# Optimization experiments

Measured on AMD Instinct MI355X. Metric: run time of the kernel, lower is better.

The kernel has to match this reference:

```python
import jax, jax.numpy as jnp
import numpy as np

KL_W = 0.001
Q_W = 0.1

def setup_inputs() -> dict:
    key = jax.random.key(0)
    k1, k2, k3, k4 = jax.random.split(key, 4)
    B, N, M, L = 2, 4096, 4096, 512
    return {
        'pred': jax.random.normal(k1, (B, N, 3), dtype=jnp.float32),
        'target': jax.random.normal(k2, (B, M, 3), dtype=jnp.float32),
        'mu': jax.random.normal(k3, (B, L), dtype=jnp.float32),
        'logvar': jax.random.normal(k4, (B, L), dtype=jnp.float32),
    }

def reference(pred, target, mu, logvar):
    # Chamfer distance: pairwise squared distances [B, N, M] then min-reductions
    d_pt = jnp.sum((pred[:, :, None, :] - target[:, None, :, :]) ** 2, axis=-1)
    cd = (d_pt.min(axis=2).mean(axis=1) + d_pt.min(axis=1).mean(axis=1)).mean()

    # KL divergence of diagonal Gaussian vs standard normal
    kl = -0.5 * jnp.mean(1.0 + logvar - mu ** 2 - jnp.exp(logvar))

    # Density uniformity: nearest-neighbor self-distance std (unbiased, like torch.std)
    d_pp = jnp.sum((pred[:, :, None, :] - pred[:, None, :, :]) ** 2, axis=-1)
    N = pred.shape[1]
    d_pp = d_pp + jnp.eye(N, dtype=pred.dtype)[None] * 1e6  # mask self-distance
    nn_dist = d_pp.min(axis=2)  # [B, N]
    density = jnp.std(nn_dist, axis=1, ddof=1).mean()

    total = cd + KL_W * kl + Q_W * density
    return total, cd, kl, density
```

## Files before the change

kernel.cpp:

```cpp
#include <hip/hip_runtime.h>
#include <hip/hip_bf16.h>
#include <math.h>

constexpr int B = 2;
constexpr int N = 4096;
constexpr int M = 4096;
constexpr int L = 512;

constexpr float KL_W = 0.001f;
constexpr float Q_W  = 0.1f;

constexpr int THREADS = 256;
constexpr int QPT     = 4;
constexpr int QC      = THREADS * QPT;
constexpr int DT      = 128;
constexpr int GX      = N / QC;
constexpr int GY      = M / DT;
constexpr int GZ      = 3 * B;

constexpr size_t OFF_PARTIAL = 0;
constexpr size_t OFF_BSUMS   = (size_t)GY * GZ * N * 4;

__global__ __launch_bounds__(THREADS) void mgl_pairmin_kernel(
    const float* __restrict__ pred, const float* __restrict__ target,
    float* __restrict__ partial)
{
    __shared__ float4 tile[DT];

    const int z   = blockIdx.z;
    const int dir = z >> 1;
    const int b   = z & 1;

    const float* qb; const float* db;
    if (dir == 0)      { qb = pred   + b * N * 3; db = target + b * M * 3; }
    else if (dir == 1) { qb = target + b * M * 3; db = pred   + b * N * 3; }
    else               { qb = pred   + b * N * 3; db = pred   + b * N * 3; }

    const int q0 = blockIdx.x * QC;
    const int d0 = blockIdx.y * DT;

    if (threadIdx.x < DT) {
        const float* p = db + (size_t)(d0 + threadIdx.x) * 3;
        float x = p[0], y = p[1], zz = p[2];
        tile[threadIdx.x] = make_float4(x, y, zz, fmaf(x, x, fmaf(y, y, zz * zz)));
    }

    int   qi[QPT];
    float ax[QPT], ay[QPT], az[QPT], qw[QPT], m[QPT];
    #pragma unroll
    for (int k = 0; k < QPT; ++k) {
        qi[k] = q0 + threadIdx.x + k * THREADS;
        float x = qb[qi[k] * 3 + 0], y = qb[qi[k] * 3 + 1], zz = qb[qi[k] * 3 + 2];
        qw[k] = fmaf(x, x, fmaf(y, y, zz * zz));
        ax[k] = -2.0f * x; ay[k] = -2.0f * y; az[k] = -2.0f * zz;
        m[k]  = 3.402823466e+38f;
    }

    __syncthreads();

    const bool diag = (dir == 2) && (d0 < q0 + QC) && (d0 + DT > q0);

    if (!diag) {
        #pragma unroll 8
        for (int j = 0; j < DT; ++j) {
            float4 t = tile[j];
            #pragma unroll
            for (int k = 0; k < QPT; ++k) {
                float v = fmaf(ax[k], t.x, fmaf(ay[k], t.y, fmaf(az[k], t.z, t.w)));
                m[k] = fminf(m[k], v);
            }
        }
    } else {
        #pragma unroll 8
        for (int j = 0; j < DT; ++j) {
            float4 t = tile[j];
            const int dj = d0 + j;
            #pragma unroll
            for (int k = 0; k < QPT; ++k) {
                float v = fmaf(ax[k], t.x, fmaf(ay[k], t.y, fmaf(az[k], t.z, t.w)));
                v = (dj == qi[k]) ? 3.402823466e+38f : v;
                m[k] = fminf(m[k], v);
            }
        }
    }

    float* slice = partial + ((size_t)blockIdx.y * GZ + z) * N;
    #pragma unroll
    for (int k = 0; k < QPT; ++k)
        slice[qi[k]] = fmaxf(m[k] + qw[k], 0.0f);
}

__global__ __launch_bounds__(256) void mgl_reduce_kernel(
    const float* __restrict__ partial, double* __restrict__ blocksums)
{
    const int tid = threadIdx.x;
    const int bid = blockIdx.x;
    const int z   = bid >> 2;
    const int q4  = ((bid & 3) * 256 + tid) * 4;

    const float4* p = (const float4*)(partial + (size_t)z * N + q4);
    float4 m = p[0];
    #pragma unroll
    for (int gy = 1; gy < GY; ++gy) {
        float4 v = p[(size_t)gy * (GZ * N / 4)];
        m.x = fminf(m.x, v.x); m.y = fminf(m.y, v.y);
        m.z = fminf(m.z, v.z); m.w = fminf(m.w, v.w);
    }

    double s  = (double)m.x + (double)m.y + (double)m.z + (double)m.w;
    double ss = (double)m.x * m.x + (double)m.y * m.y
              + (double)m.z * m.z + (double)m.w * m.w;

    #pragma unroll
    for (int off = 32; off > 0; off >>= 1) {
        s  += __shfl_down(s,  off, 64);
        ss += __shfl_down(ss, off, 64);
    }
    __shared__ double wred[4][2];
    const int wid  = tid >> 6;
    const int lane = tid & 63;
    if (lane == 0) { wred[wid][0] = s; wred[wid][1] = ss; }
    __syncthreads();
    if (tid == 0) {
        double ts  = wred[0][0] + wred[1][0] + wred[2][0] + wred[3][0];
        double tss = wred[0][1] + wred[1][1] + wred[2][1] + wred[3][1];
        blocksums[bid * 2 + 0] = ts;
        blocksums[bid * 2 + 1] = tss;
    }
}

__global__ __launch_bounds__(256) void mgl_final_kernel(
    const double* __restrict__ blocksums, const float* __restrict__ mu,
    const float* __restrict__ logvar, float* __restrict__ out)
{
    const int tid = threadIdx.x;

    double skl = 0.0;
    #pragma unroll
    for (int k = 0; k < 4; ++k) {
        int i = tid * 4 + k;
        double m  = (double)mu[i];
        double lv = (double)logvar[i];
        skl += 1.0 + lv - m * m - exp(lv);
    }
    #pragma unroll
    for (int off = 32; off > 0; off >>= 1)
        skl += __shfl_down(skl, off, 64);

    __shared__ double wkl[4];
    const int wid  = tid >> 6;
    const int lane = tid & 63;
    if (lane == 0) wkl[wid] = skl;
    __syncthreads();

    if (tid == 0) {
        double tkl = wkl[0] + wkl[1] + wkl[2] + wkl[3];

        double sPT[B] = {0.0, 0.0}, sTP[B] = {0.0, 0.0};
        double sPP[B] = {0.0, 0.0}, ssPP[B] = {0.0, 0.0};
        for (int bid = 0; bid < 24; ++bid) {
            const int z   = bid >> 2;
            const int dir = z >> 1;
            const int bb  = z & 1;
            double s  = blocksums[bid * 2 + 0];
            double ss = blocksums[bid * 2 + 1];
            if (dir == 0)      sPT[bb] += s;
            else if (dir == 1) sTP[bb] += s;
            else             { sPP[bb] += s; ssPP[bb] += ss; }
        }

        double cd = 0.0;
        #pragma unroll
        for (int bb = 0; bb < B; ++bb)
            cd += sPT[bb] / (double)N + sTP[bb] / (double)M;
        cd /= (double)B;

        double density = 0.0;
        #pragma unroll
        for (int bb = 0; bb < B; ++bb) {
            double s  = sPP[bb];
            double ss = ssPP[bb];
            double var = (ss - s * s / (double)N) / (double)(N - 1);
            density += sqrt(var > 0.0 ? var : 0.0);
        }
        density /= (double)B;

        double kl = -0.5 * tkl / (double)(B * L);

        double total = cd + (double)KL_W * kl + (double)Q_W * density;
        out[0] = (float)total;
        out[1] = (float)cd;
        out[2] = (float)kl;
        out[3] = (float)density;
    }
}

extern "C" void kernel_launch(void* const* d_in, const int* in_sizes, int n_in,
                              void* d_out, int out_size, void* d_ws, size_t ws_size,
                              hipStream_t stream) {
    const float* pred   = (const float*)d_in[0];
    const float* target = (const float*)d_in[1];
    const float* mu     = (const float*)d_in[2];
    const float* logvar = (const float*)d_in[3];
    float* out = (float*)d_out;

    char* ws = (char*)d_ws;
    float*  partial   = (float*)(ws + OFF_PARTIAL);
    double* blocksums = (double*)(ws + OFF_BSUMS);

    mgl_pairmin_kernel<<<dim3(GX, GY, GZ), THREADS, 0, stream>>>(pred, target, partial);
    mgl_reduce_kernel<<<24, 256, 0, stream>>>(partial, blocksums);
    mgl_final_kernel<<<1, 256, 0, stream>>>(blocksums, mu, logvar, out);
}
```

Baseline: 75.23 us.

## Retile pairwise-min with full query ownership per block and fuse reduce/final kernels

Each block now covers all 4096 queries (512 threads × 8 queries) against a 32-point data tile, giving 128×6 blocks instead of 4×32×6. The diagonal self-distance mask is moved out of the hot loop into a small per-thread fix-up pass. The reduce and final kernels are merged with a last-block-done atomic counter, which removes one launch. In exchange the partial buffer grows four times larger (128 slices), so the reduce pass reads more memory, and per-thread register pressure goes up.

```diff
diff --git a/kernel.cpp b/kernel.cpp
--- a/kernel.cpp
+++ b/kernel.cpp
@@ -1,5 +1,4 @@
 #include <hip/hip_runtime.h>
-#include <hip/hip_bf16.h>
 #include <math.h>
 
 constexpr int B = 2;
@@ -10,163 +9,161 @@
 constexpr float KL_W = 0.001f;
 constexpr float Q_W  = 0.1f;
 
-constexpr int THREADS = 256;
-constexpr int QPT     = 4;
+constexpr int THREADS = 512;
+constexpr int QPT     = 8;
 constexpr int QC      = THREADS * QPT;
-constexpr int DT      = 128;
-constexpr int GX      = N / QC;
+constexpr int DT      = 32;
 constexpr int GY      = M / DT;
 constexpr int GZ      = 3 * B;
+constexpr int RB      = 96;
 
 constexpr size_t OFF_PARTIAL = 0;
 constexpr size_t OFF_BSUMS   = (size_t)GY * GZ * N * 4;
+constexpr size_t OFF_CTR     = OFF_BSUMS + (size_t)RB * 2 * 8;
 
 __global__ __launch_bounds__(THREADS) void mgl_pairmin_kernel(
     const float* __restrict__ pred, const float* __restrict__ target,
-    float* __restrict__ partial)
+    float* __restrict__ partial, int* __restrict__ ctr)
 {
     __shared__ float4 tile[DT];
 
-    const int z   = blockIdx.z;
+    const int tid = threadIdx.x;
+    const int z   = blockIdx.y;
     const int dir = z >> 1;
     const int b   = z & 1;
+
+    if (blockIdx.x == 0 && z == 0 && tid == 0) *ctr = 0;
 
     const float* qb; const float* db;
     if (dir == 0)      { qb = pred   + b * N * 3; db = target + b * M * 3; }
     else if (dir == 1) { qb = target + b * M * 3; db = pred   + b * N * 3; }
     else               { qb = pred   + b * N * 3; db = pred   + b * N * 3; }
 
-    const int q0 = blockIdx.x * QC;
-    const int d0 = blockIdx.y * DT;
-
-    if (threadIdx.x < DT) {
-        const float* p = db + (size_t)(d0 + threadIdx.x) * 3;
+    const int d0 = blockIdx.x * DT;
+
+    if (tid < DT) {
+        const float* p = db + (size_t)(d0 + tid) * 3;
         float x = p[0], y = p[1], zz = p[2];
-        tile[threadIdx.x] = make_float4(x, y, zz, fmaf(x, x, fmaf(y, y, zz * zz)));
-    }
-
-    int   qi[QPT];
+        tile[tid] = make_float4(x, y, zz, fmaf(x, x, fmaf(y, y, zz * zz)));
+    }
+
     float ax[QPT], ay[QPT], az[QPT], qw[QPT], m[QPT];
+    int kb = -1, jb = 0;
     #pragma unroll
     for (int k = 0; k < QPT; ++k) {
-        qi[k] = q0 + threadIdx.x + k * THREADS;
-        float x = qb[qi[k] * 3 + 0], y = qb[qi[k] * 3 + 1], zz = qb[qi[k] * 3 + 2];
+        const int qk = tid + k * THREADS;
+        const float* p = qb + (size_t)qk * 3;
+        float x = p[0], y = p[1], zz = p[2];
         qw[k] = fmaf(x, x, fmaf(y, y, zz * zz));
         ax[k] = -2.0f * x; ay[k] = -2.0f * y; az[k] = -2.0f * zz;
         m[k]  = 3.402823466e+38f;
+        const int j = qk - d0;
+        if (dir == 2 && (unsigned)j < (unsigned)DT) { kb = k; jb = j; }
     }
 
     __syncthreads();
 
-    const bool diag = (dir == 2) && (d0 < q0 + QC) && (d0 + DT > q0);
-
-    if (!diag) {
-        #pragma unroll 8
+    #pragma unroll 4
+    for (int j = 0; j < DT; j += 2) {
+        float4 t0 = tile[j];
+        float4 t1 = tile[j + 1];
+        #pragma unroll
+        for (int k = 0; k < QPT; ++k) {
+            float v0 = fmaf(ax[k], t0.x, fmaf(ay[k], t0.y, fmaf(az[k], t0.z, t0.w)));
+            float v1 = fmaf(ax[k], t1.x, fmaf(ay[k], t1.y, fmaf(az[k], t1.z, t1.w)));
+            m[k] = fminf(fminf(m[k], v0), v1);
+        }
+    }
+
+    if (kb >= 0) {
+        float bx = 0.f, by = 0.f, bz = 0.f;
+        #pragma unroll
+        for (int k = 0; k < QPT; ++k)
+            if (k == kb) { bx = ax[k]; by = ay[k]; bz = az[k]; }
+        float mm = 3.402823466e+38f;
+        #pragma unroll 4
         for (int j = 0; j < DT; ++j) {
             float4 t = tile[j];
-            #pragma unroll
-            for (int k = 0; k < QPT; ++k) {
-                float v = fmaf(ax[k], t.x, fmaf(ay[k], t.y, fmaf(az[k], t.z, t.w)));
-                m[k] = fminf(m[k], v);
-            }
-        }
-    } else {
-        #pragma unroll 8
-        for (int j = 0; j < DT; ++j) {
-            float4 t = tile[j];
-            const int dj = d0 + j;
-            #pragma unroll
-            for (int k = 0; k < QPT; ++k) {
-                float v = fmaf(ax[k], t.x, fmaf(ay[k], t.y, fmaf(az[k], t.z, t.w)));
-                v = (dj == qi[k]) ? 3.402823466e+38f : v;
-                m[k] = fminf(m[k], v);
-            }
-        }
-    }
-
-    float* slice = partial + ((size_t)blockIdx.y * GZ + z) * N;
+            float v = fmaf(bx, t.x, fmaf(by, t.y, fmaf(bz, t.z, t.w)));
+            mm = (j == jb) ? mm : fminf(mm, v);
+        }
+        #pragma unroll
+        for (int k = 0; k < QPT; ++k)
+            if (k == kb) m[k] = mm;
+    }
+
+    float* slice = partial + ((size_t)blockIdx.x * GZ + z) * N;
     #pragma unroll
     for (int k = 0; k < QPT; ++k)
-        slice[qi[k]] = fmaxf(m[k] + qw[k], 0.0f);
+        slice[tid + k * THREADS] = fmaxf(m[k] + qw[k], 0.0f);
 }
 
-__global__ __launch_bounds__(256) void mgl_reduce_kernel(
-    const float* __restrict__ partial, double* __restrict__ blocksums)
+__global__ __launch_bounds__(64) void mgl_reduce_final_kernel(
+    const float* __restrict__ partial, const float* __restrict__ mu,
+    const float* __restrict__ logvar, double* __restrict__ blocksums,
+    int* __restrict__ ctr, float* __restrict__ out)
 {
     const int tid = threadIdx.x;
     const int bid = blockIdx.x;
-    const int z   = bid >> 2;
-    const int q4  = ((bid & 3) * 256 + tid) * 4;
-
-    const float4* p = (const float4*)(partial + (size_t)z * N + q4);
-    float4 m = p[0];
-    #pragma unroll
+    const int z   = bid >> 4;
+    const int idx = ((bid & 15) << 6) | tid;
+
+    constexpr size_t SL = (size_t)GZ * N / 4;
+    const float4* p = (const float4*)(partial + (size_t)z * N) + idx;
+
+    float4 mn = p[0];
+    #pragma unroll 8
     for (int gy = 1; gy < GY; ++gy) {
-        float4 v = p[(size_t)gy * (GZ * N / 4)];
-        m.x = fminf(m.x, v.x); m.y = fminf(m.y, v.y);
-        m.z = fminf(m.z, v.z); m.w = fminf(m.w, v.w);
-    }
-
-    double s  = (double)m.x + (double)m.y + (double)m.z + (double)m.w;
-    double ss = (double)m.x * m.x + (double)m.y * m.y
-              + (double)m.z * m.z + (double)m.w * m.w;
+        float4 v = p[(size_t)gy * SL];
+        mn.x = fminf(mn.x, v.x); mn.y = fminf(mn.y, v.y);
+        mn.z = fminf(mn.z, v.z); mn.w = fminf(mn.w, v.w);
+    }
+
+    double s  = (double)mn.x + (double)mn.y + (double)mn.z + (double)mn.w;
+    double ss = (double)mn.x * mn.x + (double)mn.y * mn.y
+              + (double)mn.z * mn.z + (double)mn.w * mn.w;
 
     #pragma unroll
     for (int off = 32; off > 0; off >>= 1) {
         s  += __shfl_down(s,  off, 64);
         ss += __shfl_down(ss, off, 64);
     }
-    __shared__ double wred[4][2];
-    const int wid  = tid >> 6;
-    const int lane = tid & 63;
-    if (lane == 0) { wred[wid][0] = s; wred[wid][1] = ss; }
-    __syncthreads();
+
+    int lastf = 0;
     if (tid == 0) {
-        double ts  = wred[0][0] + wred[1][0] + wred[2][0] + wred[3][0];
-        double tss = wred[0][1] + wred[1][1] + wred[2][1] + wred[3][1];
-        blocksums[bid * 2 + 0] = ts;
-        blocksums[bid * 2 + 1] = tss;
-    }
-}
-
-__global__ __launch_bounds__(256) void mgl_final_kernel(
-    const double* __restrict__ blocksums, const float* __restrict__ mu,
-    const float* __restrict__ logvar, float* __restrict__ out)
-{
-    const int tid = threadIdx.x;
+        blocksums[bid * 2 + 0] = s;
+        blocksums[bid * 2 + 1] = ss;
+        __threadfence();
+        lastf = (atomicAdd(ctr, 1) == RB - 1);
+    }
+    lastf = __shfl(lastf, 0, 64);
+    if (!lastf) return;
+    __threadfence();
 
     double skl = 0.0;
     #pragma unroll
-    for (int k = 0; k < 4; ++k) {
-        int i = tid * 4 + k;
-        double m  = (double)mu[i];
+    for (int k = 0; k < (B * L) / 64; ++k) {
+        const int i = (k << 6) | tid;
+        double mm = (double)mu[i];
         double lv = (double)logvar[i];
-        skl += 1.0 + lv - m * m - exp(lv);
+        skl += 1.0 + lv - mm * mm - exp(lv);
     }
     #pragma unroll
     for (int off = 32; off > 0; off >>= 1)
         skl += __shfl_down(skl, off, 64);
 
-    __shared__ double wkl[4];
-    const int wid  = tid >> 6;
-    const int lane = tid & 63;
-    if (lane == 0) wkl[wid] = skl;
-    __syncthreads();
-
     if (tid == 0) {
-        double tkl = wkl[0] + wkl[1] + wkl[2] + wkl[3];
-
         double sPT[B] = {0.0, 0.0}, sTP[B] = {0.0, 0.0};
         double sPP[B] = {0.0, 0.0}, ssPP[B] = {0.0, 0.0};
-        for (int bid = 0; bid < 24; ++bid) {
-            const int z   = bid >> 2;
-            const int dir = z >> 1;
-            const int bb  = z & 1;
-            double s  = blocksums[bid * 2 + 0];
-            double ss = blocksums[bid * 2 + 1];
-            if (dir == 0)      sPT[bb] += s;
-            else if (dir == 1) sTP[bb] += s;
-            else             { sPP[bb] += s; ssPP[bb] += ss; }
+        for (int i = 0; i < RB; ++i) {
+            const int zz  = i >> 4;
+            const int dr  = zz >> 1;
+            const int bb  = zz & 1;
+            double s_  = blocksums[i * 2 + 0];
+            double ss_ = blocksums[i * 2 + 1];
+            if (dr == 0)      sPT[bb] += s_;
+            else if (dr == 1) sTP[bb] += s_;
+            else            { sPP[bb] += s_; ssPP[bb] += ss_; }
         }
 
         double cd = 0.0;
@@ -178,14 +175,12 @@
         double density = 0.0;
         #pragma unroll
         for (int bb = 0; bb < B; ++bb) {
-            double s  = sPP[bb];
-            double ss = ssPP[bb];
-            double var = (ss - s * s / (double)N) / (double)(N - 1);
+            double var = (ssPP[bb] - sPP[bb] * sPP[bb] / (double)N) / (double)(N - 1);
             density += sqrt(var > 0.0 ? var : 0.0);
         }
         density /= (double)B;
 
-        double kl = -0.5 * tkl / (double)(B * L);
+        double kl = -0.5 * skl / (double)(B * L);
 
         double total = cd + (double)KL_W * kl + (double)Q_W * density;
         out[0] = (float)total;
@@ -207,8 +202,8 @@
     char* ws = (char*)d_ws;
     float*  partial   = (float*)(ws + OFF_PARTIAL);
     double* blocksums = (double*)(ws + OFF_BSUMS);
-
-    mgl_pairmin_kernel<<<dim3(GX, GY, GZ), THREADS, 0, stream>>>(pred, target, partial);
-    mgl_reduce_kernel<<<24, 256, 0, stream>>>(partial, blocksums);
-    mgl_final_kernel<<<1, 256, 0, stream>>>(blocksums, mu, logvar, out);
+    int*    ctr       = (int*)(ws + OFF_CTR);
+
+    mgl_pairmin_kernel<<<dim3(GY, GZ), THREADS, 0, stream>>>(pred, target, partial, ctr);
+    mgl_reduce_final_kernel<<<RB, 64, 0, stream>>>(partial, mu, logvar, blocksums, ctr, out);
 }
```

Result: slower. 99.08 us (+31.7%).
